# Kernel optimization log

Hardware: AMD Instinct MI355X
Metric: run time of the kernel (lower is better)

The kernel has to match this reference:

```python
import jax, jax.numpy as jnp
import numpy as np

N_NODES = 100000
N_EDGES = 3200000
N_FEAT = 128
N_GRAPHS = 512


def setup_inputs() -> dict:
    key = jax.random.key(0)
    ks = jax.random.split(key, 12)
    x = jax.random.normal(ks[0], (N_NODES, N_FEAT), dtype=jnp.float32)
    edge_index = jax.random.randint(ks[1], (2, N_EDGES), 0, N_NODES, dtype=jnp.int64)
    batch = jnp.sort(jax.random.randint(ks[2], (N_NODES,), 0, N_GRAPHS, dtype=jnp.int64))
    s = 0.1
    return {
        "x": x,
        "edge_index": edge_index,
        "batch": batch,
        "W1": jax.random.normal(ks[3], (N_FEAT, 64), dtype=jnp.float32) * s,
        "b1": jnp.zeros((64,), dtype=jnp.float32),
        "W2": jax.random.normal(ks[4], (64, 64), dtype=jnp.float32) * s,
        "b2": jnp.zeros((64,), dtype=jnp.float32),
        "Wl1": jax.random.normal(ks[5], (64, 32), dtype=jnp.float32) * s,
        "bl1": jnp.zeros((32,), dtype=jnp.float32),
        "Wl2": jax.random.normal(ks[6], (32, 2), dtype=jnp.float32) * s,
        "bl2": jnp.zeros((2,), dtype=jnp.float32),
    }


def gcn_conv(x, src, dst, W, b, n_nodes):
    # PyG GCNConv: linear transform first, then symmetric-normalized
    # aggregation over A + I (self loops), bias added after aggregation.
    h = x @ W  # [N, out]
    loop = jnp.arange(n_nodes, dtype=src.dtype)
    s = jnp.concatenate([src, loop])
    d = jnp.concatenate([dst, loop])
    deg = jax.ops.segment_sum(jnp.ones(d.shape, dtype=h.dtype), d, num_segments=n_nodes)
    dinv = jax.lax.rsqrt(jnp.where(deg > 0, deg, 1.0))
    norm = dinv[s] * dinv[d]  # [E+N]
    msg = h[s] * norm[:, None]  # gather + scale
    out = jax.ops.segment_sum(msg, d, num_segments=n_nodes)  # scatter-add
    return out + b


def reference(x, edge_index, batch, W1, b1, W2, b2, Wl1, bl1, Wl2, bl2):
    src, dst = edge_index[0], edge_index[1]
    h = jax.nn.relu(gcn_conv(x, src, dst, W1, b1, N_NODES))
    # dropout is identity in eval mode
    h = gcn_conv(h, src, dst, W2, b2, N_NODES)
    # global mean pool over graphs
    counts = jax.ops.segment_sum(jnp.ones((N_NODES,), dtype=h.dtype), batch, num_segments=N_GRAPHS)
    pooled = jax.ops.segment_sum(h, batch, num_segments=N_GRAPHS)
    pooled = pooled / jnp.maximum(counts, 1.0)[:, None]  # [G, 64]
    z = pooled @ Wl1 + bl1
    z = z @ Wl2 + bl2  # [G, 2]
    return jax.nn.softmax(z, axis=0)  # faithful to Softmax(dim=0)
```

## Files before the change

### kernel.cpp

```cpp
#include <hip/hip_runtime.h>
#include <hip/hip_fp16.h>
#include <math.h>

#define N_NODES 100000
#define N_EDGES 3200000
#define N_GRAPHS 512

#define BSHIFT 8
#define BSPAN 256
#define NB 391
#define SBLK 4096
#define SBLOCKS ((N_EDGES + SBLK - 1) / SBLK)
#define SCAN_IT ((SBLOCKS + 255) / 256)

typedef float floatx2 __attribute__((ext_vector_type(2)));

__global__ __launch_bounds__(256) void phist_kernel(const int* __restrict__ dst,
                                                    int* __restrict__ pcnt, int E) {
    __shared__ int h[NB];
    int tid = threadIdx.x;
    for (int b = tid; b < NB; b += 256) h[b] = 0;
    __syncthreads();
    int base = blockIdx.x * SBLK;
    int end = min(E, base + SBLK);
    for (int e = base + tid; e < end; e += 256)
        atomicAdd(&h[dst[e] >> BSHIFT], 1);
    __syncthreads();
    int* row = pcnt + (size_t)blockIdx.x * NB;
    for (int b = tid; b < NB; b += 256) row[b] = h[b];
}

__global__ __launch_bounds__(256) void pscanA_kernel(int* __restrict__ pcnt,
                                                     int* __restrict__ btot) {
    __shared__ int s[256];
    int b = blockIdx.x, tid = threadIdx.x;
    int v[SCAN_IT];
    int sum = 0;
#pragma unroll
    for (int j = 0; j < SCAN_IT; ++j) {
        int idx = tid * SCAN_IT + j;
        v[j] = (idx < SBLOCKS) ? pcnt[(size_t)idx * NB + b] : 0;
        sum += v[j];
    }
    s[tid] = sum;
    __syncthreads();
    for (int st = 1; st < 256; st <<= 1) {
        int t = (tid >= st) ? s[tid - st] : 0;
        __syncthreads();
        s[tid] += t;
        __syncthreads();
    }
    int run = s[tid] - sum;
#pragma unroll
    for (int j = 0; j < SCAN_IT; ++j) {
        int idx = tid * SCAN_IT + j;
        if (idx < SBLOCKS) pcnt[(size_t)idx * NB + b] = run;
        run += v[j];
    }
    if (tid == 255) btot[b] = run;
}

__global__ __launch_bounds__(512) void pscanB_kernel(const int* __restrict__ btot,
                                                     int* __restrict__ bbase,
                                                     int* __restrict__ offN, int E) {
    __shared__ int s[512];
    int tid = threadIdx.x;
    int v = (tid < NB) ? btot[tid] : 0;
    s[tid] = v;
    __syncthreads();
    for (int st = 1; st < 512; st <<= 1) {
        int t = (tid >= st) ? s[tid - st] : 0;
        __syncthreads();
        s[tid] += t;
        __syncthreads();
    }
    int excl = s[tid] - v;
    if (tid < NB) bbase[tid] = excl;
    if (tid == NB - 1) bbase[NB] = excl + v;
    if (tid == 0) *offN = E;
}

__global__ __launch_bounds__(256) void scatter2_kernel(const int* __restrict__ src,
                                                       const int* __restrict__ dst,
                                                       const int* __restrict__ pbase,
                                                       const int* __restrict__ bbase,
                                                       unsigned int* __restrict__ pairs, int E) {
    __shared__ int hrank[NB];
    __shared__ int hb[NB];
    int tid = threadIdx.x;
    const int* row = pbase + (size_t)blockIdx.x * NB;
    for (int b = tid; b < NB; b += 256) { hrank[b] = 0; hb[b] = row[b] + bbase[b]; }
    __syncthreads();
    int base = blockIdx.x * SBLK;
    int end = min(E, base + SBLK);
    for (int e = base + tid; e < end; e += 256) {
        int d = dst[e];
        int b = d >> BSHIFT;
        int rk = atomicAdd(&hrank[b], 1);
        pairs[hb[b] + rk] = ((unsigned int)src[e] << BSHIFT) | (unsigned int)(d & (BSPAN - 1));
    }
}

__global__ __launch_bounds__(256) void bucket_kernel(const unsigned int* __restrict__ pairs,
                                                     const int* __restrict__ bbase,
                                                     int* __restrict__ col,
                                                     int* __restrict__ off,
                                                     float* __restrict__ dinv, int N) {
    __shared__ int ncnt[BSPAN];
    __shared__ int nbase[BSPAN];
    __shared__ int a[BSPAN];
    int b = blockIdx.x, tid = threadIdx.x;
    int base = bbase[b];
    int cntb = bbase[b + 1] - base;
    int n0 = b << BSHIFT;
    int nn = min(BSPAN, N - n0);
    ncnt[tid] = 0;
    __syncthreads();
    for (int i = tid; i < cntb; i += 256)
        atomicAdd(&ncnt[pairs[base + i] & (BSPAN - 1)], 1);
    __syncthreads();
    int v = ncnt[tid];
    a[tid] = v;
    __syncthreads();
    for (int st = 1; st < 256; st <<= 1) {
        int t = (tid >= st) ? a[tid - st] : 0;
        __syncthreads();
        a[tid] += t;
        __syncthreads();
    }
    nbase[tid] = a[tid] - v;
    if (tid < nn) {
        off[n0 + tid] = base + nbase[tid];
        dinv[n0 + tid] = rsqrtf((float)(v + 1));
    }
    ncnt[tid] = 0;
    __syncthreads();
    for (int i = tid; i < cntb; i += 256) {
        unsigned int p = pairs[base + i];
        int dl = p & (BSPAN - 1);
        int pos = base + nbase[dl] + atomicAdd(&ncnt[dl], 1);
        col[pos] = (int)(p >> BSHIFT) << 3;
    }
}

__global__ __launch_bounds__(128) void wz_kernel(const float* __restrict__ W2,
                                                 const float* __restrict__ b2,
                                                 const float* __restrict__ Wl1,
                                                 const float* __restrict__ bl1,
                                                 const float* __restrict__ Wl2,
                                                 const float* __restrict__ bl2,
                                                 float* __restrict__ Wz,
                                                 float* __restrict__ zc) {
    __shared__ float Weff[64 * 2];
    int tid = threadIdx.x;
    {
        int c = tid >> 1, j = tid & 1;
        float s = 0.f;
        for (int k = 0; k < 32; ++k) s += Wl1[c * 32 + k] * Wl2[k * 2 + j];
        Weff[c * 2 + j] = s;
    }
    __syncthreads();
    {
        int i = tid >> 1, j = tid & 1;
        float s = 0.f;
        for (int c = 0; c < 64; ++c) s += W2[i * 64 + c] * Weff[c * 2 + j];
        Wz[i * 2 + j] = s;
    }
    if (tid < 2) {
        float s = bl2[tid];
        for (int k = 0; k < 32; ++k) s += bl1[k] * Wl2[k * 2 + tid];
        for (int c = 0; c < 64; ++c) s += b2[c] * Weff[c * 2 + tid];
        zc[tid] = s;
    }
}

template <int K>
__global__ __launch_bounds__(256) void lin_kernel(const float* __restrict__ X,
                                                  const float* __restrict__ W,
                                                  const float* __restrict__ rs,
                                                  unsigned char* __restrict__ U) {
    __shared__ float Ws[K * 64];
    __shared__ float Xs[32 * K];
    int tid = threadIdx.x;
    for (int i = tid * 4; i < K * 64; i += 256 * 4)
        *reinterpret_cast<float4*>(&Ws[i]) = *reinterpret_cast<const float4*>(&W[i]);
    int row0 = blockIdx.x * 32;
    const float* Xbase = X + (size_t)row0 * K;
    for (int i = tid * 4; i < 32 * K; i += 256 * 4)
        *reinterpret_cast<float4*>(&Xs[i]) = *reinterpret_cast<const float4*>(&Xbase[i]);
    __syncthreads();

    int wid = tid >> 6, lane = tid & 63;
    int rbase = wid * 8;
    float acc[8];
#pragma unroll
    for (int r = 0; r < 8; ++r) acc[r] = 0.f;

    for (int k4 = 0; k4 < K / 4; ++k4) {
        float w0 = Ws[(k4 * 4 + 0) * 64 + lane];
        float w1 = Ws[(k4 * 4 + 1) * 64 + lane];
        float w2 = Ws[(k4 * 4 + 2) * 64 + lane];
        float w3 = Ws[(k4 * 4 + 3) * 64 + lane];
#pragma unroll
        for (int r = 0; r < 8; ++r) {
            float4 xv = *reinterpret_cast<const float4*>(&Xs[(rbase + r) * K + k4 * 4]);
            acc[r] += xv.x * w0 + xv.y * w1 + xv.z * w2 + xv.w * w3;
        }
    }
#pragma unroll
    for (int r = 0; r < 8; ++r) {
        int row = row0 + rbase + r;
        float v = acc[r] * rs[row];
        int pk = __builtin_amdgcn_cvt_pk_fp8_f32(v, v, 0, false);
        U[(size_t)row * 64 + lane] = (unsigned char)(pk & 0xff);
    }
}

#define ACC8(a)                                                                  \
    {                                                                            \
        floatx2 f_;                                                              \
        f_ = __builtin_amdgcn_cvt_pk_f32_fp8((int)(a).x, false);                 \
        acc[0] += f_.x; acc[1] += f_.y;                                          \
        f_ = __builtin_amdgcn_cvt_pk_f32_fp8((int)(a).x, true);                  \
        acc[2] += f_.x; acc[3] += f_.y;                                          \
        f_ = __builtin_amdgcn_cvt_pk_f32_fp8((int)(a).y, false);                 \
        acc[4] += f_.x; acc[5] += f_.y;                                          \
        f_ = __builtin_amdgcn_cvt_pk_f32_fp8((int)(a).y, true);                  \
        acc[6] += f_.x; acc[7] += f_.y;                                          \
    }

__global__ __launch_bounds__(256) void agg1_kernel(const unsigned char* __restrict__ u,
                                                   const int* __restrict__ off,
                                                   const int* __restrict__ col,
                                                   const float* __restrict__ dinv,
                                                   const float* __restrict__ bias,
                                                   const float* __restrict__ Wz,
                                                   float2* __restrict__ qz, int n) {
    __shared__ float Wzs[128];
    int tid = threadIdx.x;
    if (tid < 128) Wzs[tid] = Wz[tid];
    __syncthreads();

    int wid = tid >> 6, lane = tid & 63;
    int node = blockIdx.x * 4 + wid;
    if (node >= n) return;
    int r = lane >> 3, c = lane & 7;
    unsigned int c8 = (unsigned int)c * 8;

    int beg = off[node], end = off[node + 1];
    float acc[8];
#pragma unroll
    for (int j = 0; j < 8; ++j) acc[j] = 0.f;
    int e = beg + r;
    while (e + 24 < end) {
        unsigned int v0 = ((unsigned int)col[e]      << 3) + c8;
        unsigned int v1 = ((unsigned int)col[e + 8]  << 3) + c8;
        unsigned int v2 = ((unsigned int)col[e + 16] << 3) + c8;
        unsigned int v3 = ((unsigned int)col[e + 24] << 3) + c8;
        uint2 a0 = *reinterpret_cast<const uint2*>(u + v0);
        uint2 a1 = *reinterpret_cast<const uint2*>(u + v1);
        uint2 a2 = *reinterpret_cast<const uint2*>(u + v2);
        uint2 a3 = *reinterpret_cast<const uint2*>(u + v3);
        ACC8(a0); ACC8(a1); ACC8(a2); ACC8(a3);
        e += 32;
    }
    while (e + 8 < end) {
        unsigned int v0 = ((unsigned int)col[e]     << 3) + c8;
        unsigned int v1 = ((unsigned int)col[e + 8] << 3) + c8;
        uint2 a0 = *reinterpret_cast<const uint2*>(u + v0);
        uint2 a1 = *reinterpret_cast<const uint2*>(u + v1);
        ACC8(a0); ACC8(a1);
        e += 16;
    }
    if (e < end) {
        unsigned int v0 = ((unsigned int)col[e] << 3) + c8;
        uint2 a0 = *reinterpret_cast<const uint2*>(u + v0);
        ACC8(a0);
    }
#pragma unroll
    for (int m = 8; m <= 32; m <<= 1) {
#pragma unroll
        for (int j = 0; j < 8; ++j) acc[j] += __shfl_xor(acc[j], m);
    }
    unsigned int vs = ((unsigned int)node << 6) + c8;
    uint2 sfr = *reinterpret_cast<const uint2*>(u + vs);
    ACC8(sfr);
    float di = dinv[node];
    float4 b0 = *reinterpret_cast<const float4*>(&bias[c * 8]);
    float4 b1 = *reinterpret_cast<const float4*>(&bias[c * 8 + 4]);
    float o[8];
#pragma unroll
    for (int j = 0; j < 8; ++j) o[j] = di * acc[j];
    o[0] += b0.x; o[1] += b0.y; o[2] += b0.z; o[3] += b0.w;
    o[4] += b1.x; o[5] += b1.y; o[6] += b1.z; o[7] += b1.w;
#pragma unroll
    for (int j = 0; j < 8; ++j) o[j] = fmaxf(o[j], 0.f);
    float p0 = 0.f, p1 = 0.f;
#pragma unroll
    for (int j = 0; j < 8; ++j) {
        p0 += o[j] * Wzs[(c * 8 + j) * 2 + 0];
        p1 += o[j] * Wzs[(c * 8 + j) * 2 + 1];
    }
#pragma unroll
    for (int m = 1; m <= 4; m <<= 1) {
        p0 += __shfl_xor(p0, m);
        p1 += __shfl_xor(p1, m);
    }
    if (lane == 0) qz[node] = make_float2(p0 * di, p1 * di);
}

__global__ __launch_bounds__(256) void agg2q_kernel(const float2* __restrict__ qz,
                                                    const int* __restrict__ off,
                                                    const int* __restrict__ col,
                                                    const float* __restrict__ dinv,
                                                    float* __restrict__ pooled2,
                                                    const int* __restrict__ batch, int n) {
    __shared__ float2 sh[16];
    __shared__ int sg[16];
    int tid = threadIdx.x;
    int wid = tid >> 6, lane = tid & 63;
    int sub = lane >> 4, slot = lane & 15;
    int li = wid * 4 + sub;
    int node = blockIdx.x * 16 + li;
    bool valid = node < n;

    float ax = 0.f, ay = 0.f;
    if (valid) {
        int beg = off[node], end = off[node + 1];
        const char* qb = (const char*)qz;
        int e = beg + slot;
        while (e + 16 < end) {
            float2 v0 = *reinterpret_cast<const float2*>(qb + (unsigned int)col[e]);
            float2 v1 = *reinterpret_cast<const float2*>(qb + (unsigned int)col[e + 16]);
            ax += v0.x + v1.x; ay += v0.y + v1.y;
            e += 32;
        }
        if (e < end) {
            float2 v0 = *reinterpret_cast<const float2*>(qb + (unsigned int)col[e]);
            ax += v0.x; ay += v0.y;
        }
    }
#pragma unroll
    for (int m = 1; m <= 8; m <<= 1) {
        ax += __shfl_xor(ax, m);
        ay += __shfl_xor(ay, m);
    }
    if (slot == 0) {
        if (valid) {
            float2 self = qz[node];
            float di = dinv[node];
            sh[li] = make_float2(di * (ax + self.x), di * (ay + self.y));
            sg[li] = batch[node];
        } else {
            sh[li] = make_float2(0.f, 0.f);
            sg[li] = -1;
        }
    }
    __syncthreads();
    if (tid < 2) {
        float s = 0.f;
        int gp = -1;
        for (int w = 0; w < 16; ++w) {
            int g = sg[w];
            if (g < 0) continue;
            if (g != gp) {
                if (gp >= 0) atomicAdd(&pooled2[gp * 2 + tid], s);
                s = 0.f;
                gp = g;
            }
            s += (tid == 0) ? sh[w].x : sh[w].y;
        }
        if (gp >= 0) atomicAdd(&pooled2[gp * 2 + tid], s);
    }
}

__global__ __launch_bounds__(512) void head_kernel(const float* __restrict__ pooled2,
                                                   const int* __restrict__ batch,
                                                   const float* __restrict__ zc,
                                                   float* __restrict__ out, int N) {
    __shared__ float red[512];
    int tid = threadIdx.x;
    int g = tid;
    auto lb = [&](int key) {
        int l = 0, r = N;
        while (l < r) { int m = (l + r) >> 1; if (batch[m] < key) l = m + 1; else r = m; }
        return l;
    };
    int cnt = lb(g + 1) - lb(g);
    float cn = fmaxf((float)cnt, 1.f);
    float z0 = pooled2[g * 2 + 0] / cn + zc[0];
    float z1 = pooled2[g * 2 + 1] / cn + zc[1];

    red[tid] = z0; __syncthreads();
    for (int s = 256; s > 0; s >>= 1) { if (tid < s) red[tid] = fmaxf(red[tid], red[tid + s]); __syncthreads(); }
    float m0 = red[0]; __syncthreads();
    float e0 = expf(z0 - m0);
    red[tid] = e0; __syncthreads();
    for (int s = 256; s > 0; s >>= 1) { if (tid < s) red[tid] += red[tid + s]; __syncthreads(); }
    float s0 = red[0]; __syncthreads();
    out[g * 2 + 0] = e0 / s0;

    red[tid] = z1; __syncthreads();
    for (int s = 256; s > 0; s >>= 1) { if (tid < s) red[tid] = fmaxf(red[tid], red[tid + s]); __syncthreads(); }
    float m1 = red[0]; __syncthreads();
    float e1 = expf(z1 - m1);
    red[tid] = e1; __syncthreads();
    for (int s = 256; s > 0; s >>= 1) { if (tid < s) red[tid] += red[tid + s]; __syncthreads(); }
    float s1 = red[0]; __syncthreads();
    out[g * 2 + 1] = e1 / s1;
}

extern "C" void kernel_launch(void* const* d_in, const int* in_sizes, int n_in,
                              void* d_out, int out_size, void* d_ws, size_t ws_size,
                              hipStream_t stream) {
    const float* x   = (const float*)d_in[0];
    const int*   ei  = (const int*)d_in[1];
    const int*   bat = (const int*)d_in[2];
    const float* W1  = (const float*)d_in[3];
    const float* b1  = (const float*)d_in[4];
    const float* W2  = (const float*)d_in[5];
    const float* b2  = (const float*)d_in[6];
    const float* Wl1 = (const float*)d_in[7];
    const float* bl1 = (const float*)d_in[8];
    const float* Wl2 = (const float*)d_in[9];
    const float* bl2 = (const float*)d_in[10];
    float* out = (float*)d_out;

    const int N = N_NODES, E = N_EDGES;
    const int* src = ei;
    const int* dst = ei + E;

    size_t o = 0;
    auto alloc = [&](size_t bytes) {
        void* p = (char*)d_ws + o;
        o += (bytes + 255) / 256 * 256;
        return p;
    };
    int*           pcnt    = (int*)alloc((size_t)SBLOCKS * NB * 4);
    int*           btot    = (int*)alloc((size_t)NB * 4);
    int*           bbase   = (int*)alloc((size_t)(NB + 1) * 4);
    int*           off     = (int*)alloc((size_t)(N + 1) * 4);
    float*         dinv    = (float*)alloc((size_t)N * 4);
    unsigned int*  pairs   = (unsigned int*)alloc((size_t)E * 4);
    int*           col     = (int*)alloc((size_t)E * 4);
    unsigned char* T       = (unsigned char*)alloc((size_t)N * 64);
    float2*        qz      = (float2*)alloc((size_t)N * 8);
    float*         Wz      = (float*)alloc(128 * 4);
    float*         zc      = (float*)alloc(2 * 4);
    float*         pooled2 = (float*)alloc((size_t)N_GRAPHS * 2 * 4);

    hipMemsetAsync(pooled2, 0, (size_t)N_GRAPHS * 2 * 4, stream);

    phist_kernel<<<SBLOCKS, 256, 0, stream>>>(dst, pcnt, E);
    pscanA_kernel<<<NB, 256, 0, stream>>>(pcnt, btot);
    pscanB_kernel<<<1, 512, 0, stream>>>(btot, bbase, off + N, E);
    scatter2_kernel<<<SBLOCKS, 256, 0, stream>>>(src, dst, pcnt, bbase, pairs, E);
    bucket_kernel<<<NB, 256, 0, stream>>>(pairs, bbase, col, off, dinv, N);

    wz_kernel<<<1, 128, 0, stream>>>(W2, b2, Wl1, bl1, Wl2, bl2, Wz, zc);

    lin_kernel<128><<<N / 32, 256, 0, stream>>>(x, W1, dinv, T);
    agg1_kernel<<<(N + 3) / 4, 256, 0, stream>>>(T, off, col, dinv, b1, Wz, qz, N);

    agg2q_kernel<<<(N + 15) / 16, 256, 0, stream>>>(qz, off, col, dinv, pooled2, bat, N);

    head_kernel<<<1, 512, 0, stream>>>(pooled2, bat, zc, out, N);
}
```

Baseline: 225.7 us.

## Vectorize edge loads in histogram/scatter and pack fp8 accumulation in agg1

The partition histogram and scatter kernels now have each thread load four dst (and src) indices per int4 load, replacing one scalar load per edge. This cuts load instruction count, but the per-thread access pattern becomes strided. The agg1 kernel accumulates decoded fp8 pairs into packed float2 vectors so the adds can use packed instructions. It also restricts the epilogue to one row of lanes and splits Wz into two contiguous shared arrays. The shuffle in the epilogue now runs under a divergent branch, which stays correct because the lanes involved all share r==0.

```diff
diff --git a/kernel.cpp b/kernel.cpp
--- a/kernel.cpp
+++ b/kernel.cpp
@@ -23,8 +23,15 @@
     __syncthreads();
     int base = blockIdx.x * SBLK;
     int end = min(E, base + SBLK);
-    for (int e = base + tid; e < end; e += 256)
-        atomicAdd(&h[dst[e] >> BSHIFT], 1);
+    int e = base + tid * 4;
+    for (; e + 3 < end; e += 1024) {
+        int4 d4 = *reinterpret_cast<const int4*>(&dst[e]);
+        atomicAdd(&h[d4.x >> BSHIFT], 1);
+        atomicAdd(&h[d4.y >> BSHIFT], 1);
+        atomicAdd(&h[d4.z >> BSHIFT], 1);
+        atomicAdd(&h[d4.w >> BSHIFT], 1);
+    }
+    for (; e < end; ++e) atomicAdd(&h[dst[e] >> BSHIFT], 1);
     __syncthreads();
     int* row = pcnt + (size_t)blockIdx.x * NB;
     for (int b = tid; b < NB; b += 256) row[b] = h[b];
@@ -93,7 +100,21 @@
     __syncthreads();
     int base = blockIdx.x * SBLK;
     int end = min(E, base + SBLK);
-    for (int e = base + tid; e < end; e += 256) {
+    int e = base + tid * 4;
+    for (; e + 3 < end; e += 1024) {
+        int4 d4 = *reinterpret_cast<const int4*>(&dst[e]);
+        int4 s4 = *reinterpret_cast<const int4*>(&src[e]);
+        int b0 = d4.x >> BSHIFT, b1 = d4.y >> BSHIFT, b2 = d4.z >> BSHIFT, b3 = d4.w >> BSHIFT;
+        int r0 = atomicAdd(&hrank[b0], 1);
+        int r1 = atomicAdd(&hrank[b1], 1);
+        int r2 = atomicAdd(&hrank[b2], 1);
+        int r3 = atomicAdd(&hrank[b3], 1);
+        pairs[hb[b0] + r0] = ((unsigned int)s4.x << BSHIFT) | (unsigned int)(d4.x & (BSPAN - 1));
+        pairs[hb[b1] + r1] = ((unsigned int)s4.y << BSHIFT) | (unsigned int)(d4.y & (BSPAN - 1));
+        pairs[hb[b2] + r2] = ((unsigned int)s4.z << BSHIFT) | (unsigned int)(d4.z & (BSPAN - 1));
+        pairs[hb[b3] + r3] = ((unsigned int)s4.w << BSHIFT) | (unsigned int)(d4.w & (BSPAN - 1));
+    }
+    for (; e < end; ++e) {
         int d = dst[e];
         int b = d >> BSHIFT;
         int rk = atomicAdd(&hrank[b], 1);
@@ -218,15 +239,10 @@
 
 #define ACC8(a)                                                                  \
     {                                                                            \
-        floatx2 f_;                                                              \
-        f_ = __builtin_amdgcn_cvt_pk_f32_fp8((int)(a).x, false);                 \
-        acc[0] += f_.x; acc[1] += f_.y;                                          \
-        f_ = __builtin_amdgcn_cvt_pk_f32_fp8((int)(a).x, true);                  \
-        acc[2] += f_.x; acc[3] += f_.y;                                          \
-        f_ = __builtin_amdgcn_cvt_pk_f32_fp8((int)(a).y, false);                 \
-        acc[4] += f_.x; acc[5] += f_.y;                                          \
-        f_ = __builtin_amdgcn_cvt_pk_f32_fp8((int)(a).y, true);                  \
-        acc[6] += f_.x; acc[7] += f_.y;                                          \
+        acc2[0] += __builtin_amdgcn_cvt_pk_f32_fp8((int)(a).x, false);           \
+        acc2[1] += __builtin_amdgcn_cvt_pk_f32_fp8((int)(a).x, true);            \
+        acc2[2] += __builtin_amdgcn_cvt_pk_f32_fp8((int)(a).y, false);           \
+        acc2[3] += __builtin_amdgcn_cvt_pk_f32_fp8((int)(a).y, true);            \
     }
 
 __global__ __launch_bounds__(256) void agg1_kernel(const unsigned char* __restrict__ u,
@@ -236,9 +252,11 @@
                                                    const float* __restrict__ bias,
                                                    const float* __restrict__ Wz,
                                                    float2* __restrict__ qz, int n) {
-    __shared__ float Wzs[128];
-    int tid = threadIdx.x;
-    if (tid < 128) Wzs[tid] = Wz[tid];
+    __shared__ float Wz0s[64];
+    __shared__ float Wz1s[64];
+    int tid = threadIdx.x;
+    if (tid < 64) Wz0s[tid] = Wz[tid * 2];
+    else if (tid < 128) Wz1s[tid - 64] = Wz[(tid - 64) * 2 + 1];
     __syncthreads();
 
     int wid = tid >> 6, lane = tid & 63;
@@ -248,9 +266,9 @@
     unsigned int c8 = (unsigned int)c * 8;
 
     int beg = off[node], end = off[node + 1];
-    float acc[8];
-#pragma unroll
-    for (int j = 0; j < 8; ++j) acc[j] = 0.f;
+    floatx2 acc2[4];
+#pragma unroll
+    for (int j = 0; j < 4; ++j) acc2[j] = (floatx2)(0.f);
     int e = beg + r;
     while (e + 24 < end) {
         unsigned int v0 = ((unsigned int)col[e]      << 3) + c8;
@@ -280,33 +298,41 @@
 #pragma unroll
     for (int m = 8; m <= 32; m <<= 1) {
 #pragma unroll
-        for (int j = 0; j < 8; ++j) acc[j] += __shfl_xor(acc[j], m);
-    }
-    unsigned int vs = ((unsigned int)node << 6) + c8;
-    uint2 sfr = *reinterpret_cast<const uint2*>(u + vs);
-    ACC8(sfr);
-    float di = dinv[node];
-    float4 b0 = *reinterpret_cast<const float4*>(&bias[c * 8]);
-    float4 b1 = *reinterpret_cast<const float4*>(&bias[c * 8 + 4]);
-    float o[8];
-#pragma unroll
-    for (int j = 0; j < 8; ++j) o[j] = di * acc[j];
-    o[0] += b0.x; o[1] += b0.y; o[2] += b0.z; o[3] += b0.w;
-    o[4] += b1.x; o[5] += b1.y; o[6] += b1.z; o[7] += b1.w;
-#pragma unroll
-    for (int j = 0; j < 8; ++j) o[j] = fmaxf(o[j], 0.f);
-    float p0 = 0.f, p1 = 0.f;
-#pragma unroll
-    for (int j = 0; j < 8; ++j) {
-        p0 += o[j] * Wzs[(c * 8 + j) * 2 + 0];
-        p1 += o[j] * Wzs[(c * 8 + j) * 2 + 1];
-    }
-#pragma unroll
-    for (int m = 1; m <= 4; m <<= 1) {
-        p0 += __shfl_xor(p0, m);
-        p1 += __shfl_xor(p1, m);
-    }
-    if (lane == 0) qz[node] = make_float2(p0 * di, p1 * di);
+        for (int j = 0; j < 4; ++j) {
+            acc2[j].x += __shfl_xor(acc2[j].x, m);
+            acc2[j].y += __shfl_xor(acc2[j].y, m);
+        }
+    }
+    if (r == 0) {
+        unsigned int vs = ((unsigned int)node << 6) + c8;
+        uint2 sfr = *reinterpret_cast<const uint2*>(u + vs);
+        ACC8(sfr);
+        float di = dinv[node];
+        float4 b0 = *reinterpret_cast<const float4*>(&bias[c * 8]);
+        float4 b1 = *reinterpret_cast<const float4*>(&bias[c * 8 + 4]);
+        float o[8];
+#pragma unroll
+        for (int j = 0; j < 4; ++j) {
+            o[2 * j]     = di * acc2[j].x;
+            o[2 * j + 1] = di * acc2[j].y;
+        }
+        o[0] += b0.x; o[1] += b0.y; o[2] += b0.z; o[3] += b0.w;
+        o[4] += b1.x; o[5] += b1.y; o[6] += b1.z; o[7] += b1.w;
+#pragma unroll
+        for (int j = 0; j < 8; ++j) o[j] = fmaxf(o[j], 0.f);
+        float p0 = 0.f, p1 = 0.f;
+#pragma unroll
+        for (int j = 0; j < 8; ++j) {
+            p0 += o[j] * Wz0s[c * 8 + j];
+            p1 += o[j] * Wz1s[c * 8 + j];
+        }
+#pragma unroll
+        for (int m = 1; m <= 4; m <<= 1) {
+            p0 += __shfl_xor(p0, m);
+            p1 += __shfl_xor(p1, m);
+        }
+        if (lane == 0) qz[node] = make_float2(p0 * di, p1 * di);
+    }
 }
 
 __global__ __launch_bounds__(256) void agg2q_kernel(const float2* __restrict__ qz,
```

Measured after the change: 216.8 us. -3.9%, faster.
